# Kernel tuning notes

Hardware: AMD Instinct MI355X
Metric: run time of the kernel (lower is better)

The kernel has to match this reference:

```python
import jax, jax.numpy as jnp
import numpy as np

N, F_IN, F_OUT = 1024, 128, 128
NEG_SLOPE = 0.01  # F.leaky_relu default


def setup_inputs() -> dict:
    key = jax.random.key(0)
    ks = jax.random.split(key, 6)
    return {
        "V": jax.random.normal(ks[0], (N, F_IN), jnp.float32),
        "E": jax.random.uniform(ks[1], (N, N), jnp.float32),
        "time_enc": jax.random.normal(ks[2], (N, N, F_IN), jnp.float32),
        "W_weight": jax.random.normal(ks[3], (F_OUT, F_IN), jnp.float32) * 0.05,
        "W_bias": jax.random.normal(ks[4], (F_OUT,), jnp.float32) * 0.05,
        "a": jax.random.normal(ks[5], (2 * F_OUT + F_IN, 1), jnp.float32),
    }


def reference(V, E, time_enc, W_weight, W_bias, a):
    # Project node features ONCE (original redundantly projects N-repeated tensors)
    Vp = V @ W_weight.T + W_bias            # [N, F'] == W(V)
    av = a[:, 0]
    a_i, a_j, a_t = av[:F_OUT], av[F_OUT:2 * F_OUT], av[2 * F_OUT:]
    # cat([W(V_i), W(V_j), time_enc]) @ a  ==  (Wp V_i).a_i + (Wp V_j).a_j + time_enc.a_t
    s_i = Vp @ a_i                          # [N] contribution from i (row)
    s_j = Vp @ a_j                          # [N] contribution from j (col)
    score = s_i[:, None] + s_j[None, :] + jnp.einsum('ijf,f->ij', time_enc, a_t)  # [N, N]
    score = jax.nn.leaky_relu(score, NEG_SLOPE)
    att = jax.nn.softmax(score, axis=-1)    # softmax over j
    # H = att * M * E, with M = W(V_j) broadcast over rows
    H = att[:, :, None] * Vp[None, :, :] * E[:, :, None]  # [N, N, F']
    return H
```

## Files before the change

kernel.cpp:

```cpp
#include <hip/hip_runtime.h>
#include <hip/hip_bf16.h>
#include <math.h>

#define N 1024
#define F 128
#define NEG_SLOPE 0.01f

typedef float f32x4 __attribute__((ext_vector_type(4)));

__global__ __launch_bounds__(128) void gat_prep(
    const float* __restrict__ V,
    const float* __restrict__ W,
    const float* __restrict__ b,
    const float* __restrict__ a,
    float* __restrict__ Vp,
    float* __restrict__ s_i,
    float* __restrict__ s_j)
{
    const int i = blockIdx.x;
    const int f = threadIdx.x;
    __shared__ float vsh[F];
    vsh[f] = V[i * F + f];
    __syncthreads();

    const float* wrow = W + f * F;
    float acc = b[f];
#pragma unroll 4
    for (int k = 0; k < F; ++k) acc += vsh[k] * wrow[k];
    Vp[(size_t)i * F + f] = acc;

    float pi = acc * a[f];
    float pj = acc * a[F + f];
#pragma unroll
    for (int off = 32; off; off >>= 1) {
        pi += __shfl_xor(pi, off, 64);
        pj += __shfl_xor(pj, off, 64);
    }
    __shared__ float r[4];
    if ((f & 63) == 0) { r[(f >> 6) * 2 + 0] = pi; r[(f >> 6) * 2 + 1] = pj; }
    __syncthreads();
    if (f == 0) { s_i[i] = r[0] + r[2]; s_j[i] = r[1] + r[3]; }
}

__global__ __launch_bounds__(512, 8) void gat_main(
    const float* __restrict__ time_enc,
    const float* __restrict__ E,
    const float* __restrict__ Vp,
    const float* __restrict__ s_i,
    const float* __restrict__ s_j,
    const float* __restrict__ a_t,
    float* __restrict__ H)
{
    const int i    = blockIdx.x;
    const int tid  = threadIdx.x;
    const int wave = tid >> 6;
    const int lane = tid & 63;
    const int half = lane >> 5;
    const int hl   = lane & 31;

    __shared__ float sc[N];
    __shared__ float sjs[N];
    __shared__ float Esh[N];
    __shared__ float red[16];

    const float* Erow = E + (size_t)i * N;
    for (int j = tid; j < N; j += 512) { sjs[j] = s_j[j]; Esh[j] = Erow[j]; }

    const f32x4 at4 = *reinterpret_cast<const f32x4*>(a_t + 4 * hl);
    const float si  = s_i[i];
    const float* te_row = time_enc + (size_t)i * N * F;
    __syncthreads();

    float lmax = -INFINITY;
    for (int jb = wave * 4; jb < N; jb += 32) {
        const f32x4 t0 = __builtin_nontemporal_load(
            reinterpret_cast<const f32x4*>(te_row + (size_t)(jb + half) * F + 4 * hl));
        const f32x4 t1 = __builtin_nontemporal_load(
            reinterpret_cast<const f32x4*>(te_row + (size_t)(jb + 2 + half) * F + 4 * hl));
        float d0 = t0.x * at4.x + t0.y * at4.y + t0.z * at4.z + t0.w * at4.w;
        float d1 = t1.x * at4.x + t1.y * at4.y + t1.z * at4.z + t1.w * at4.w;
#pragma unroll
        for (int off = 16; off; off >>= 1) {
            d0 += __shfl_xor(d0, off, 64);
            d1 += __shfl_xor(d1, off, 64);
        }
        if (hl == 0) {
            float s0 = si + sjs[jb + half] + d0;
            float s1 = si + sjs[jb + 2 + half] + d1;
            s0 = (s0 > 0.f) ? s0 : NEG_SLOPE * s0;
            s1 = (s1 > 0.f) ? s1 : NEG_SLOPE * s1;
            sc[jb + half] = s0;
            sc[jb + 2 + half] = s1;
            lmax = fmaxf(lmax, fmaxf(s0, s1));
        }
    }
    lmax = fmaxf(lmax, __shfl_xor(lmax, 32, 64));
    if (lane == 0) red[wave] = lmax;
    __syncthreads();
    float m = red[0];
#pragma unroll
    for (int w = 1; w < 8; ++w) m = fmaxf(m, red[w]);

    float lsum = 0.f;
    for (int j = tid; j < N; j += 512) {
        float e = __expf(sc[j] - m);
        sc[j] = e;
        lsum += e;
    }
#pragma unroll
    for (int off = 32; off; off >>= 1) lsum += __shfl_xor(lsum, off, 64);
    if (lane == 0) red[8 + wave] = lsum;
    __syncthreads();
    float tot = red[8];
#pragma unroll
    for (int w = 1; w < 8; ++w) tot += red[8 + w];
    const float inv = 1.f / tot;

    float* Hrow = H + (size_t)i * N * F;
    for (int jb = wave * 4; jb < N; jb += 32) {
        const f32x4 v0 = *reinterpret_cast<const f32x4*>(Vp + (size_t)(jb + half) * F + 4 * hl);
        const f32x4 v1 = *reinterpret_cast<const f32x4*>(Vp + (size_t)(jb + 2 + half) * F + 4 * hl);
        const float k0 = sc[jb + half] * inv * Esh[jb + half];
        const float k1 = sc[jb + 2 + half] * inv * Esh[jb + 2 + half];
        *reinterpret_cast<f32x4*>(Hrow + (size_t)(jb + half) * F + 4 * hl) = v0 * k0;
        *reinterpret_cast<f32x4*>(Hrow + (size_t)(jb + 2 + half) * F + 4 * hl) = v1 * k1;
    }
}

extern "C" void kernel_launch(void* const* d_in, const int* in_sizes, int n_in,
                              void* d_out, int out_size, void* d_ws, size_t ws_size,
                              hipStream_t stream) {
    const float* V  = (const float*)d_in[0];
    const float* E  = (const float*)d_in[1];
    const float* TE = (const float*)d_in[2];
    const float* W  = (const float*)d_in[3];
    const float* Wb = (const float*)d_in[4];
    const float* a  = (const float*)d_in[5];

    float* H = (float*)d_out;

    float* Vp  = (float*)d_ws;
    float* s_i = Vp + (size_t)N * F;
    float* s_j = s_i + N;

    gat_prep<<<N, 128, 0, stream>>>(V, W, Wb, a, Vp, s_i, s_j);
    gat_main<<<N, 512, 0, stream>>>(TE, E, Vp, s_i, s_j, a + 2 * F, H);
}
```

Baseline: 197.9 us.

## Process two rows per block, overlapping row A output writes with row B score reads

Result: slower. 216.9 us (+9.6%).

```diff
diff --git a/kernel.cpp b/kernel.cpp
--- a/kernel.cpp
+++ b/kernel.cpp
@@ -51,32 +51,40 @@
     const float* __restrict__ a_t,
     float* __restrict__ H)
 {
-    const int i    = blockIdx.x;
+    const int iA   = 2 * blockIdx.x;
+    const int iB   = iA + 1;
     const int tid  = threadIdx.x;
     const int wave = tid >> 6;
     const int lane = tid & 63;
     const int half = lane >> 5;
     const int hl   = lane & 31;
 
-    __shared__ float sc[N];
+    __shared__ float scA[N], scB[N];
     __shared__ float sjs[N];
-    __shared__ float Esh[N];
+    __shared__ float EshA[N], EshB[N];
     __shared__ float red[16];
 
-    const float* Erow = E + (size_t)i * N;
-    for (int j = tid; j < N; j += 512) { sjs[j] = s_j[j]; Esh[j] = Erow[j]; }
+    for (int j = tid; j < N; j += 512) {
+        sjs[j]  = s_j[j];
+        EshA[j] = E[(size_t)iA * N + j];
+        EshB[j] = E[(size_t)iB * N + j];
+    }
 
     const f32x4 at4 = *reinterpret_cast<const f32x4*>(a_t + 4 * hl);
-    const float si  = s_i[i];
-    const float* te_row = time_enc + (size_t)i * N * F;
+    const float siA = s_i[iA];
+    const float siB = s_i[iB];
+    const float* teA = time_enc + (size_t)iA * N * F;
+    const float* teB = time_enc + (size_t)iB * N * F;
+    float* HrowA = H + (size_t)iA * N * F;
+    float* HrowB = H + (size_t)iB * N * F;
     __syncthreads();
 
     float lmax = -INFINITY;
     for (int jb = wave * 4; jb < N; jb += 32) {
         const f32x4 t0 = __builtin_nontemporal_load(
-            reinterpret_cast<const f32x4*>(te_row + (size_t)(jb + half) * F + 4 * hl));
+            reinterpret_cast<const f32x4*>(teA + (size_t)(jb + half) * F + 4 * hl));
         const f32x4 t1 = __builtin_nontemporal_load(
-            reinterpret_cast<const f32x4*>(te_row + (size_t)(jb + 2 + half) * F + 4 * hl));
+            reinterpret_cast<const f32x4*>(teA + (size_t)(jb + 2 + half) * F + 4 * hl));
         float d0 = t0.x * at4.x + t0.y * at4.y + t0.z * at4.z + t0.w * at4.w;
         float d1 = t1.x * at4.x + t1.y * at4.y + t1.z * at4.z + t1.w * at4.w;
 #pragma unroll
@@ -85,45 +93,97 @@
             d1 += __shfl_xor(d1, off, 64);
         }
         if (hl == 0) {
-            float s0 = si + sjs[jb + half] + d0;
-            float s1 = si + sjs[jb + 2 + half] + d1;
+            float s0 = siA + sjs[jb + half] + d0;
+            float s1 = siA + sjs[jb + 2 + half] + d1;
             s0 = (s0 > 0.f) ? s0 : NEG_SLOPE * s0;
             s1 = (s1 > 0.f) ? s1 : NEG_SLOPE * s1;
-            sc[jb + half] = s0;
-            sc[jb + 2 + half] = s1;
+            scA[jb + half] = s0;
+            scA[jb + 2 + half] = s1;
             lmax = fmaxf(lmax, fmaxf(s0, s1));
         }
     }
     lmax = fmaxf(lmax, __shfl_xor(lmax, 32, 64));
     if (lane == 0) red[wave] = lmax;
     __syncthreads();
-    float m = red[0];
-#pragma unroll
-    for (int w = 1; w < 8; ++w) m = fmaxf(m, red[w]);
+    float mA = red[0];
+#pragma unroll
+    for (int w = 1; w < 8; ++w) mA = fmaxf(mA, red[w]);
 
     float lsum = 0.f;
     for (int j = tid; j < N; j += 512) {
-        float e = __expf(sc[j] - m);
-        sc[j] = e;
+        float e = __expf(scA[j] - mA);
+        scA[j] = e;
         lsum += e;
     }
 #pragma unroll
     for (int off = 32; off; off >>= 1) lsum += __shfl_xor(lsum, off, 64);
     if (lane == 0) red[8 + wave] = lsum;
     __syncthreads();
-    float tot = red[8];
-#pragma unroll
-    for (int w = 1; w < 8; ++w) tot += red[8 + w];
-    const float inv = 1.f / tot;
-
-    float* Hrow = H + (size_t)i * N * F;
+    float totA = red[8];
+#pragma unroll
+    for (int w = 1; w < 8; ++w) totA += red[8 + w];
+    const float invA = 1.f / totA;
+
+    float lmaxB = -INFINITY;
+    for (int jb = wave * 4; jb < N; jb += 32) {
+        const f32x4 t0 = __builtin_nontemporal_load(
+            reinterpret_cast<const f32x4*>(teB + (size_t)(jb + half) * F + 4 * hl));
+        const f32x4 t1 = __builtin_nontemporal_load(
+            reinterpret_cast<const f32x4*>(teB + (size_t)(jb + 2 + half) * F + 4 * hl));
+        const f32x4 v0 = *reinterpret_cast<const f32x4*>(Vp + (size_t)(jb + half) * F + 4 * hl);
+        const f32x4 v1 = *reinterpret_cast<const f32x4*>(Vp + (size_t)(jb + 2 + half) * F + 4 * hl);
+
+        const float kA0 = scA[jb + half] * invA * EshA[jb + half];
+        const float kA1 = scA[jb + 2 + half] * invA * EshA[jb + 2 + half];
+        *reinterpret_cast<f32x4*>(HrowA + (size_t)(jb + half) * F + 4 * hl) = v0 * kA0;
+        *reinterpret_cast<f32x4*>(HrowA + (size_t)(jb + 2 + half) * F + 4 * hl) = v1 * kA1;
+
+        float d0 = t0.x * at4.x + t0.y * at4.y + t0.z * at4.z + t0.w * at4.w;
+        float d1 = t1.x * at4.x + t1.y * at4.y + t1.z * at4.z + t1.w * at4.w;
+#pragma unroll
+        for (int off = 16; off; off >>= 1) {
+            d0 += __shfl_xor(d0, off, 64);
+            d1 += __shfl_xor(d1, off, 64);
+        }
+        if (hl == 0) {
+            float s0 = siB + sjs[jb + half] + d0;
+            float s1 = siB + sjs[jb + 2 + half] + d1;
+            s0 = (s0 > 0.f) ? s0 : NEG_SLOPE * s0;
+            s1 = (s1 > 0.f) ? s1 : NEG_SLOPE * s1;
+            scB[jb + half] = s0;
+            scB[jb + 2 + half] = s1;
+            lmaxB = fmaxf(lmaxB, fmaxf(s0, s1));
+        }
+    }
+    lmaxB = fmaxf(lmaxB, __shfl_xor(lmaxB, 32, 64));
+    if (lane == 0) red[wave] = lmaxB;
+    __syncthreads();
+    float mB = red[0];
+#pragma unroll
+    for (int w = 1; w < 8; ++w) mB = fmaxf(mB, red[w]);
+
+    float lsumB = 0.f;
+    for (int j = tid; j < N; j += 512) {
+        float e = __expf(scB[j] - mB);
+        scB[j] = e;
+        lsumB += e;
+    }
+#pragma unroll
+    for (int off = 32; off; off >>= 1) lsumB += __shfl_xor(lsumB, off, 64);
+    if (lane == 0) red[8 + wave] = lsumB;
+    __syncthreads();
+    float totB = red[8];
+#pragma unroll
+    for (int w = 1; w < 8; ++w) totB += red[8 + w];
+    const float invB = 1.f / totB;
+
     for (int jb = wave * 4; jb < N; jb += 32) {
         const f32x4 v0 = *reinterpret_cast<const f32x4*>(Vp + (size_t)(jb + half) * F + 4 * hl);
         const f32x4 v1 = *reinterpret_cast<const f32x4*>(Vp + (size_t)(jb + 2 + half) * F + 4 * hl);
-        const float k0 = sc[jb + half] * inv * Esh[jb + half];
-        const float k1 = sc[jb + 2 + half] * inv * Esh[jb + 2 + half];
-        *reinterpret_cast<f32x4*>(Hrow + (size_t)(jb + half) * F + 4 * hl) = v0 * k0;
-        *reinterpret_cast<f32x4*>(Hrow + (size_t)(jb + 2 + half) * F + 4 * hl) = v1 * k1;
+        const float kB0 = scB[jb + half] * invB * EshB[jb + half];
+        const float kB1 = scB[jb + 2 + half] * invB * EshB[jb + 2 + half];
+        *reinterpret_cast<f32x4*>(HrowB + (size_t)(jb + half) * F + 4 * hl) = v0 * kB0;
+        *reinterpret_cast<f32x4*>(HrowB + (size_t)(jb + 2 + half) * F + 4 * hl) = v1 * kB1;
     }
 }
 
@@ -144,5 +204,5 @@
     float* s_j = s_i + N;
 
     gat_prep<<<N, 128, 0, stream>>>(V, W, Wb, a, Vp, s_i, s_j);
-    gat_main<<<N, 512, 0, stream>>>(TE, E, Vp, s_i, s_j, a + 2 * F, H);
+    gat_main<<<N / 2, 512, 0, stream>>>(TE, E, Vp, s_i, s_j, a + 2 * F, H);
 }
```

## Split main kernel into score and write kernels with nontemporal H stores

Applied to the files above, without the earlier changes.

Result: no change. 196.0 us (-1.0%).

```diff
diff --git a/kernel.cpp b/kernel.cpp
--- a/kernel.cpp
+++ b/kernel.cpp
@@ -42,14 +42,13 @@
     if (f == 0) { s_i[i] = r[0] + r[2]; s_j[i] = r[1] + r[3]; }
 }
 
-__global__ __launch_bounds__(512, 8) void gat_main(
+__global__ __launch_bounds__(512, 8) void gat_score(
     const float* __restrict__ time_enc,
     const float* __restrict__ E,
-    const float* __restrict__ Vp,
     const float* __restrict__ s_i,
     const float* __restrict__ s_j,
     const float* __restrict__ a_t,
-    float* __restrict__ H)
+    float* __restrict__ kscale)
 {
     const int i    = blockIdx.x;
     const int tid  = threadIdx.x;
@@ -116,14 +115,37 @@
     for (int w = 1; w < 8; ++w) tot += red[8 + w];
     const float inv = 1.f / tot;
 
+    float* krow = kscale + (size_t)i * N;
+    for (int j = tid; j < N; j += 512) krow[j] = sc[j] * inv * Esh[j];
+}
+
+__global__ __launch_bounds__(512, 8) void gat_h(
+    const float* __restrict__ kscale,
+    const float* __restrict__ Vp,
+    float* __restrict__ H)
+{
+    const int i    = blockIdx.x;
+    const int tid  = threadIdx.x;
+    const int wave = tid >> 6;
+    const int lane = tid & 63;
+    const int half = lane >> 5;
+    const int hl   = lane & 31;
+
+    __shared__ float kk[N];
+    const float* krow = kscale + (size_t)i * N;
+    for (int j = tid; j < N; j += 512) kk[j] = krow[j];
+    __syncthreads();
+
     float* Hrow = H + (size_t)i * N * F;
     for (int jb = wave * 4; jb < N; jb += 32) {
         const f32x4 v0 = *reinterpret_cast<const f32x4*>(Vp + (size_t)(jb + half) * F + 4 * hl);
         const f32x4 v1 = *reinterpret_cast<const f32x4*>(Vp + (size_t)(jb + 2 + half) * F + 4 * hl);
-        const float k0 = sc[jb + half] * inv * Esh[jb + half];
-        const float k1 = sc[jb + 2 + half] * inv * Esh[jb + 2 + half];
-        *reinterpret_cast<f32x4*>(Hrow + (size_t)(jb + half) * F + 4 * hl) = v0 * k0;
-        *reinterpret_cast<f32x4*>(Hrow + (size_t)(jb + 2 + half) * F + 4 * hl) = v1 * k1;
+        const float k0 = kk[jb + half];
+        const float k1 = kk[jb + 2 + half];
+        __builtin_nontemporal_store(v0 * k0,
+            reinterpret_cast<f32x4*>(Hrow + (size_t)(jb + half) * F + 4 * hl));
+        __builtin_nontemporal_store(v1 * k1,
+            reinterpret_cast<f32x4*>(Hrow + (size_t)(jb + 2 + half) * F + 4 * hl));
     }
 }
 
@@ -139,10 +161,12 @@
 
     float* H = (float*)d_out;
 
-    float* Vp  = (float*)d_ws;
-    float* s_i = Vp + (size_t)N * F;
-    float* s_j = s_i + N;
+    float* Vp     = (float*)d_ws;
+    float* s_i    = Vp + (size_t)N * F;
+    float* s_j    = s_i + N;
+    float* kscale = s_j + N;
 
     gat_prep<<<N, 128, 0, stream>>>(V, W, Wb, a, Vp, s_i, s_j);
-    gat_main<<<N, 512, 0, stream>>>(TE, E, Vp, s_i, s_j, a + 2 * F, H);
+    gat_score<<<N, 512, 0, stream>>>(TE, E, s_i, s_j, a + 2 * F, kscale);
+    gat_h<<<N, 512, 0, stream>>>(kscale, Vp, H);
 }
```
